# Kernel optimization log

Hardware: AMD Instinct MI355X
Metric: run time of the kernel (lower is better)

The kernel has to match this reference:

```python
import jax, jax.numpy as jnp
import numpy as np

S, B, E = 2048, 2, 768
H = 12
D = E // H  # 64
SCALE = D ** -0.5


def setup_inputs() -> dict:
    key = jax.random.key(0)
    ks = jax.random.split(key, 10)
    inp = {
        "query": jax.random.normal(ks[0], (S, B, E), dtype=jnp.float32),
        "attn_bias": jax.random.normal(ks[1], (B * H, S, S), dtype=jnp.float32) * 0.1,
        "key_padding_mask": jax.random.randint(ks[2], (B, S), 0, 2).astype(bool),
        "Wq": jax.random.normal(ks[3], (E, E), dtype=jnp.float32) * (E ** -0.5),
        "bq": jnp.zeros((E,), dtype=jnp.float32),
        "Wk": jax.random.normal(ks[4], (E, E), dtype=jnp.float32) * (E ** -0.5),
        "bk": jnp.zeros((E,), dtype=jnp.float32),
        "Wv": jax.random.normal(ks[5], (E, E), dtype=jnp.float32) * (E ** -0.5),
        "bv": jnp.zeros((E,), dtype=jnp.float32),
        "Wo": jax.random.normal(ks[6], (E, E), dtype=jnp.float32) * (E ** -0.5),
        "bo": jnp.zeros((E,), dtype=jnp.float32),
    }
    return inp


def reference(query, attn_bias, key_padding_mask, Wq, bq, Wk, bk, Wv, bv, Wo, bo):
    s, b, e = query.shape
    # projections (torch Linear: x @ W.T + b)
    q = (query @ Wq.T + bq) * SCALE
    k = query @ Wk.T + bk
    v = query @ Wv.T + bv
    # [s, b, e] -> [b*h, s, d]
    def to_heads(x):
        return x.reshape(s, b * H, D).transpose(1, 0, 2)
    q, k, v = to_heads(q), to_heads(k), to_heads(v)
    # scores [b*h, s_q, s_k]
    scores = jnp.einsum('nqd,nkd->nqk', q, k) + attn_bias
    # key padding mask: [b, s_k] -> broadcast over heads and queries
    scores = scores.reshape(b, H, s, s)
    scores = jnp.where(key_padding_mask[:, None, None, :], -jnp.inf, scores)
    scores = scores.reshape(b * H, s, s)
    probs = jax.nn.softmax(scores, axis=-1)
    attn = jnp.einsum('nqk,nkd->nqd', probs, v)  # [b*h, s, d]
    attn = attn.transpose(1, 0, 2).reshape(s, b, e)
    return attn @ Wo.T + bo
```

## Files before the change

### kernel.cpp

```cpp
#include <hip/hip_runtime.h>
#include <hip/hip_bf16.h>

typedef __attribute__((ext_vector_type(8))) short s16x8;
typedef __attribute__((ext_vector_type(4))) float f32x4;
typedef unsigned short u16;
typedef unsigned int u32;

#define SDIM 2048
#define BDIM 2
#define HDIM 12
#define DDIM 64
#define EDIM 768
#define MDIM 4096
#define SCALE_Q 0.125f
#define KSPLIT 1024
#define NIT (KSPLIT / 32)
#define HFRAG 131072

static __device__ __forceinline__ f32x4 zero4() {
    f32x4 v; v[0] = v[1] = v[2] = v[3] = 0.f; return v;
}

static __device__ __forceinline__ u16 f2b(float x) {
    u32 u = __builtin_bit_cast(u32, x);
    u32 lsb = (u >> 16) & 1u;
    u += 0x7fffu + lsb;
    return (u16)(u >> 16);
}

static __device__ __forceinline__ f32x4 mfma16(s16x8 a, s16x8 b, f32x4 c) {
    return __builtin_amdgcn_mfma_f32_16x16x32_bf16(a, b, c, 0, 0, 0);
}

static __device__ __forceinline__ void gload_lds16(const void* g, void* l) {
    __builtin_amdgcn_global_load_lds(
        (const __attribute__((address_space(1))) void*)g,
        (__attribute__((address_space(3))) void*)l, 16, 0, 0);
}

__global__ void mask_bits_kernel(const u32* __restrict__ raw, u32* __restrict__ outbits) {
    __shared__ int okInt, okFloat;
    int t = threadIdx.x;
    if (t == 0) { okInt = 1; okFloat = 1; }
    __syncthreads();
    int li = 1, lf = 1;
    for (int i = t; i < 1024; i += blockDim.x) {
        u32 v = raw[i];
        if (v > 1u) li = 0;
        if (v != 0u && v != 0x3F800000u) lf = 0;
    }
    if (!li) atomicAnd(&okInt, 0);
    if (!lf) atomicAnd(&okFloat, 0);
    __syncthreads();
    const unsigned char* rb = (const unsigned char*)raw;
    if (t < (BDIM * SDIM) / 32) {
        u32 bits = 0;
        for (int j = 0; j < 32; ++j) {
            int i = t * 32 + j;
            int v;
            if (okInt)        v = (int)raw[i];
            else if (okFloat) v = (raw[i] != 0u) ? 1 : 0;
            else              v = (int)rb[i];
            bits |= (v ? 1u : 0u) << j;
        }
        outbits[t] = bits;
    }
}

__global__ __launch_bounds__(256) void conv_f32_bf16(
    const float* __restrict__ s, u16* __restrict__ d, int n8)
{
    int i = blockIdx.x * 256 + threadIdx.x;
    if (i >= n8) return;
    float4 x0 = ((const float4*)s)[(size_t)i * 2];
    float4 x1 = ((const float4*)s)[(size_t)i * 2 + 1];
    uint4 o;
    o.x = (u32)f2b(x0.x) | ((u32)f2b(x0.y) << 16);
    o.y = (u32)f2b(x0.z) | ((u32)f2b(x0.w) << 16);
    o.z = (u32)f2b(x1.x) | ((u32)f2b(x1.y) << 16);
    o.w = (u32)f2b(x1.z) | ((u32)f2b(x1.w) << 16);
    ((uint4*)d)[i] = o;
}

__global__ __launch_bounds__(256) void gemm_xwT(
    const u16* __restrict__ A, const u16* __restrict__ Wb,
    const float* __restrict__ bias, float scale,
    u16* __restrict__ out_sc, float* __restrict__ out_rm, int mode)
{
    __shared__ u16 Al[64 * 56];
    __shared__ u16 Bl[64 * 56];
    int tid = threadIdx.x;
    int mb = blockIdx.x * 64, nb = blockIdx.y * 64;
    int lane = tid & 63, w = tid >> 6;
    int r16 = lane & 15, g4 = lane >> 4;
    int wm = w >> 1, wn = w & 1;

    f32x4 acc[2][2];
    acc[0][0] = zero4(); acc[0][1] = zero4(); acc[1][0] = zero4(); acc[1][1] = zero4();

    int srow = tid >> 2, scol = (tid & 3) * 8;

    for (int kb = 0; kb < EDIM; kb += 32) {
        __syncthreads();
        *(uint4*)&Al[srow * 56 + scol] =
            *(const uint4*)&A[(size_t)(mb + srow) * EDIM + kb + scol];
        *(uint4*)&Bl[srow * 56 + scol] =
            *(const uint4*)&Wb[(size_t)(nb + srow) * EDIM + kb + scol];
        __syncthreads();
        s16x8 a[2], bb[2];
        #pragma unroll
        for (int mi = 0; mi < 2; ++mi)
            a[mi] = *(const s16x8*)&Al[(wm * 32 + mi * 16 + r16) * 56 + g4 * 8];
        #pragma unroll
        for (int ni = 0; ni < 2; ++ni)
            bb[ni] = *(const s16x8*)&Bl[(wn * 32 + ni * 16 + r16) * 56 + g4 * 8];
        #pragma unroll
        for (int mi = 0; mi < 2; ++mi)
            #pragma unroll
            for (int ni = 0; ni < 2; ++ni)
                acc[mi][ni] = mfma16(a[mi], bb[ni], acc[mi][ni]);
    }

    #pragma unroll
    for (int mi = 0; mi < 2; ++mi) {
        #pragma unroll
        for (int ni = 0; ni < 2; ++ni) {
            int n = nb + wn * 32 + ni * 16 + r16;
            float bv = bias[n];
            #pragma unroll
            for (int r = 0; r < 4; ++r) {
                int m = mb + wm * 32 + mi * 16 + g4 * 4 + r;
                float c = (acc[mi][ni][r] + bv) * scale;
                if (mode == 1) {
                    int s_ = m >> 1, b_ = m & 1, h_ = n >> 6, d_ = n & 63;
                    out_sc[((size_t)(b_ * HDIM + h_) * SDIM + s_) * DDIM + d_] = f2b(c);
                } else if (mode == 3) {
                    int s_ = m >> 1, b_ = m & 1, h_ = n >> 6, d_ = n & 63;
                    size_t p = (size_t)(b_ * HDIM + h_) * HFRAG
                             + (size_t)(s_ >> 4) * 1024 + (size_t)((d_ >> 5) & 1) * 512
                             + (size_t)(((d_ >> 3) & 3) * 16 + (s_ & 15)) * 8 + (d_ & 7);
                    out_sc[p] = f2b(c);
                } else if (mode == 4) {
                    int s_ = m >> 1, b_ = m & 1, h_ = n >> 6, d_ = n & 63;
                    size_t p = (size_t)(b_ * HDIM + h_) * HFRAG
                             + (size_t)(s_ >> 5) * 2048 + (size_t)((d_ >> 4) & 3) * 512
                             + (size_t)(((s_ >> 3) & 3) * 16 + (d_ & 15)) * 8 + (s_ & 7);
                    out_sc[p] = f2b(c);
                } else {
                    out_rm[(size_t)m * EDIM + n] = c;
                }
            }
        }
    }
}

struct KV { s16x8 k0, k1, k2, k3, v0, v1, v2, v3; };

__global__ __launch_bounds__(128, 4) void attn_fused(
    const u16* __restrict__ qw, const u16* __restrict__ kf_g,
    const u16* __restrict__ vf_g, const float* __restrict__ bias,
    const u32* __restrict__ maskBits, u16* __restrict__ attn_out)
{
    __shared__ __align__(1024) unsigned char SM[18944];

    int qt = blockIdx.x, bh = blockIdx.y;
    int tid = threadIdx.x;
    int w = tid >> 6, lane = tid & 63;
    int r16 = lane & 15, g4 = lane >> 4;
    int qbase = qt * 16;
    int b_ = bh / HDIM, h_ = bh % HDIM;
    const u16* Q  = qw   + (size_t)bh * SDIM * DDIM;
    const u16* KF = kf_g + (size_t)bh * HFRAG;
    const u16* VF = vf_g + (size_t)bh * HFRAG;
    const float* BrowQ = bias + (size_t)bh * SDIM * SDIM + (size_t)qbase * SDIM;
    const u32* mB = maskBits + b_ * (SDIM / 32);

    float* BsW = (float*)(SM + w * 8192);
    u16*   Pl  = (u16*)(SM + 16384 + w * 1280);

    s16x8 qf0 = *(const s16x8*)&Q[(size_t)(qbase + r16) * DDIM + g4 * 8];
    s16x8 qf1 = *(const s16x8*)&Q[(size_t)(qbase + r16) * DDIM + g4 * 8 + 32];

    f32x4 accO[4];
    #pragma unroll
    for (int dt = 0; dt < 4; ++dt) accO[dt] = zero4();
    float m_run = -1e30f, l_run = 0.f;

    const int k0 = w * KSPLIT;

    auto issue_kv = [&](int it, KV& dst) {
        int itc = it < NIT ? it : NIT - 1;
        int kbn = k0 + itc * 32;
        const u16* KT = KF + (size_t)(kbn >> 4) * 1024;
        dst.k0 = *(const s16x8*)&KT[lane * 8];
        dst.k1 = *(const s16x8*)&KT[512 + lane * 8];
        dst.k2 = *(const s16x8*)&KT[1024 + lane * 8];
        dst.k3 = *(const s16x8*)&KT[1536 + lane * 8];
        const u16* VT = VF + (size_t)(kbn >> 5) * 2048;
        dst.v0 = *(const s16x8*)&VT[lane * 8];
        dst.v1 = *(const s16x8*)&VT[512 + lane * 8];
        dst.v2 = *(const s16x8*)&VT[1024 + lane * 8];
        dst.v3 = *(const s16x8*)&VT[1536 + lane * 8];
    };

    auto stage_bias = [&](int it) {
        int itc = it < NIT ? it : NIT - 1;
        int kb2 = k0 + itc * 32;
        float* slot = BsW + (it & 3) * 512;
        #pragma unroll
        for (int j = 0; j < 2; ++j) {
            int sl = j * 64 + lane;
            int row = sl >> 3, q8 = sl & 7;
            int sq = q8 ^ (row & 7);
            gload_lds16(&BrowQ[(size_t)row * SDIM + kb2 + sq * 4],
                        (unsigned char*)slot + j * 1024);
        }
    };

    auto compute = [&](int it, KV& cur) {
        u32 mb = mB[__builtin_amdgcn_readfirstlane((k0 + it * 32) >> 5)];
        f32x4 sc0 = mfma16(cur.k1, qf1, mfma16(cur.k0, qf0, zero4()));
        f32x4 sc1 = mfma16(cur.k3, qf1, mfma16(cur.k2, qf0, zero4()));
        float* Bs = BsW + (it & 3) * 512;
        float4 bc0 = *(const float4*)&Bs[r16 * 32 + ((g4 ^ (r16 & 7)) * 4)];
        float4 bc1 = *(const float4*)&Bs[r16 * 32 + (((4 + g4) ^ (r16 & 7)) * 4)];
        sc0[0] += bc0.x; sc0[1] += bc0.y; sc0[2] += bc0.z; sc0[3] += bc0.w;
        sc1[0] += bc1.x; sc1[1] += bc1.y; sc1[2] += bc1.z; sc1[3] += bc1.w;
        u32 h0 = mb >> (g4 * 4), h1 = mb >> (16 + g4 * 4);
        #pragma unroll
        for (int r = 0; r < 4; ++r) {
            if ((h0 >> r) & 1) sc0[r] = -1e30f;
            if ((h1 >> r) & 1) sc1[r] = -1e30f;
        }
        float pm = fmaxf(fmaxf(fmaxf(sc0[0], sc0[1]), fmaxf(sc0[2], sc0[3])),
                         fmaxf(fmaxf(sc1[0], sc1[1]), fmaxf(sc1[2], sc1[3])));
        pm = fmaxf(pm, __shfl_xor(pm, 16));
        pm = fmaxf(pm, __shfl_xor(pm, 32));
        float mn = fmaxf(m_run, pm);
        float alpha = __expf(m_run - mn);
        float p[8];
        #pragma unroll
        for (int r = 0; r < 4; ++r) p[r]     = __expf(sc0[r] - mn);
        #pragma unroll
        for (int r = 0; r < 4; ++r) p[4 + r] = __expf(sc1[r] - mn);
        float ps = ((p[0] + p[1]) + (p[2] + p[3])) + ((p[4] + p[5]) + (p[6] + p[7]));
        ps += __shfl_xor(ps, 16);
        ps += __shfl_xor(ps, 32);
        l_run = l_run * alpha + ps;
        m_run = mn;
        uint2 pv0, pv1;
        pv0.x = (u32)f2b(p[0]) | ((u32)f2b(p[1]) << 16);
        pv0.y = (u32)f2b(p[2]) | ((u32)f2b(p[3]) << 16);
        pv1.x = (u32)f2b(p[4]) | ((u32)f2b(p[5]) << 16);
        pv1.y = (u32)f2b(p[6]) | ((u32)f2b(p[7]) << 16);
        *(uint2*)&Pl[r16 * 40 + g4 * 4]      = pv0;
        *(uint2*)&Pl[r16 * 40 + 16 + g4 * 4] = pv1;
        float aR0 = __shfl(alpha, g4 * 4 + 0);
        float aR1 = __shfl(alpha, g4 * 4 + 1);
        float aR2 = __shfl(alpha, g4 * 4 + 2);
        float aR3 = __shfl(alpha, g4 * 4 + 3);
        #pragma unroll
        for (int dt = 0; dt < 4; ++dt) {
            accO[dt][0] *= aR0;
            accO[dt][1] *= aR1;
            accO[dt][2] *= aR2;
            accO[dt][3] *= aR3;
        }
        s16x8 pf = *(const s16x8*)&Pl[r16 * 40 + g4 * 8];
        accO[0] = mfma16(pf, cur.v0, accO[0]);
        accO[1] = mfma16(pf, cur.v1, accO[1]);
        accO[2] = mfma16(pf, cur.v2, accO[2]);
        accO[3] = mfma16(pf, cur.v3, accO[3]);
    };

    KV A, B;
    issue_kv(0, A);
    stage_bias(0);
    stage_bias(1);

    for (int t = 0; t < NIT; t += 2) {
        issue_kv(t + 1, B);
        stage_bias(t + 2);
        asm volatile("s_waitcnt vmcnt(12)" ::: "memory");
        __builtin_amdgcn_sched_barrier(0);
        compute(t, A);

        issue_kv(t + 2, A);
        stage_bias(t + 3);
        asm volatile("s_waitcnt vmcnt(12)" ::: "memory");
        __builtin_amdgcn_sched_barrier(0);
        compute(t + 1, B);
    }

    __syncthreads();
    float* As = (float*)SM;
    float* Ml = (float*)(SM + 8704);
    float* Ll = Ml + 32;
    #pragma unroll
    for (int dt = 0; dt < 4; ++dt)
        #pragma unroll
        for (int r = 0; r < 4; ++r)
            As[(w * 16 + g4 * 4 + r) * 68 + dt * 16 + r16] = accO[dt][r];
    if (g4 == 0) { Ml[w * 16 + r16] = m_run; Ll[w * 16 + r16] = l_run; }
    __syncthreads();

    #pragma unroll
    for (int half = 0; half < 2; ++half) {
        int d = w * 32 + half * 16 + r16;
        #pragma unroll
        for (int r = 0; r < 4; ++r) {
            int q = g4 * 4 + r;
            float m0 = Ml[q], m1 = Ml[16 + q];
            float mt = fmaxf(m0, m1);
            float e0 = __expf(m0 - mt), e1 = __expf(m1 - mt);
            float lt = Ll[q] * e0 + Ll[16 + q] * e1;
            float o = (As[q * 68 + d] * e0 + As[(16 + q) * 68 + d] * e1) / lt;
            attn_out[((size_t)(qbase + q) * BDIM + b_) * EDIM + h_ * DDIM + d] = f2b(o);
        }
    }
}

extern "C" void kernel_launch(void* const* d_in, const int* in_sizes, int n_in,
                              void* d_out, int out_size, void* d_ws, size_t ws_size,
                              hipStream_t stream) {
    const float* query     = (const float*)d_in[0];
    const float* attn_bias = (const float*)d_in[1];
    const u32*   mask_raw  = (const u32*)d_in[2];
    const float* Wq = (const float*)d_in[3];
    const float* bq = (const float*)d_in[4];
    const float* Wk = (const float*)d_in[5];
    const float* bk = (const float*)d_in[6];
    const float* Wv = (const float*)d_in[7];
    const float* bv = (const float*)d_in[8];
    const float* Wo = (const float*)d_in[9];
    const float* bo = (const float*)d_in[10];
    float* out = (float*)d_out;

    char* ws = (char*)d_ws;
    u32* maskB = (u32*)ws;
    const size_t HEADSZ = (size_t)BDIM * HDIM * SDIM * DDIM;
    const size_t WSZ = (size_t)EDIM * EDIM;
    u16* qws = (u16*)(ws + 16384);
    u16* kws = qws + HEADSZ;
    u16* vws = kws + HEADSZ;
    u16* aws = vws + HEADSZ;
    u16* qbf = aws;
    u16* wWq = aws + HEADSZ;
    u16* wWk = wWq + WSZ;
    u16* wWv = wWk + WSZ;
    u16* wWo = wWv + WSZ;

    mask_bits_kernel<<<1, 256, 0, stream>>>(mask_raw, maskB);

    conv_f32_bf16<<<(int)(MDIM * EDIM / 8 / 256), 256, 0, stream>>>(query, qbf, MDIM * EDIM / 8);
    conv_f32_bf16<<<(int)(WSZ / 8 / 256), 256, 0, stream>>>(Wq, wWq, (int)(WSZ / 8));
    conv_f32_bf16<<<(int)(WSZ / 8 / 256), 256, 0, stream>>>(Wk, wWk, (int)(WSZ / 8));
    conv_f32_bf16<<<(int)(WSZ / 8 / 256), 256, 0, stream>>>(Wv, wWv, (int)(WSZ / 8));
    conv_f32_bf16<<<(int)(WSZ / 8 / 256), 256, 0, stream>>>(Wo, wWo, (int)(WSZ / 8));

    dim3 gg(MDIM / 64, EDIM / 64);
    gemm_xwT<<<gg, 256, 0, stream>>>(qbf, wWq, bq, SCALE_Q, qws, nullptr, 1);
    gemm_xwT<<<gg, 256, 0, stream>>>(qbf, wWk, bk, 1.0f,    kws, nullptr, 3);
    gemm_xwT<<<gg, 256, 0, stream>>>(qbf, wWv, bv, 1.0f,    vws, nullptr, 4);

    dim3 ga(SDIM / 16, BDIM * HDIM);
    attn_fused<<<ga, 128, 0, stream>>>(qws, kws, vws, attn_bias, maskB, aws);

    gemm_xwT<<<gg, 256, 0, stream>>>(aws, wWo, bo, 1.0f, nullptr, out, 0);
}
```

Baseline: 257.8 us.

## Use single-wave attention blocks with 64-key steps and chunked bias ring

The attention kernel moves from two waves that each handle half the keys and merge at the end to a single wave per 16-query block that walks all keys in 64-key steps. Bias is staged into a double-buffered 256-column LDS ring, one row slice per step, and the cross-wave LDS merge and its syncthreads are removed. This aims to cut merge overhead and per-step softmax bookkeeping and to lengthen the memory pipeline. In exchange each block runs only one wave, the register footprint grows, and occupancy and latency hiding depend on many resident blocks.

```diff
diff --git a/kernel.cpp b/kernel.cpp
--- a/kernel.cpp
+++ b/kernel.cpp
@@ -13,9 +13,9 @@
 #define EDIM 768
 #define MDIM 4096
 #define SCALE_Q 0.125f
-#define KSPLIT 1024
-#define NIT (KSPLIT / 32)
 #define HFRAG 131072
+#define NBODY 32
+#define NCHUNK 8
 
 static __device__ __forceinline__ f32x4 zero4() {
     f32x4 v; v[0] = v[1] = v[2] = v[3] = 0.f; return v;
@@ -154,18 +154,18 @@
     }
 }
 
-struct KV { s16x8 k0, k1, k2, k3, v0, v1, v2, v3; };
-
-__global__ __launch_bounds__(128, 4) void attn_fused(
+struct KV { s16x8 ka[4][2]; s16x8 va[2][4]; };
+
+__global__ __launch_bounds__(64) void attn_fused(
     const u16* __restrict__ qw, const u16* __restrict__ kf_g,
     const u16* __restrict__ vf_g, const float* __restrict__ bias,
     const u32* __restrict__ maskBits, u16* __restrict__ attn_out)
 {
-    __shared__ __align__(1024) unsigned char SM[18944];
+    __shared__ float Ring[2][4096];
+    __shared__ u16 Pl[16 * 72];
 
     int qt = blockIdx.x, bh = blockIdx.y;
-    int tid = threadIdx.x;
-    int w = tid >> 6, lane = tid & 63;
+    int lane = threadIdx.x;
     int r16 = lane & 15, g4 = lane >> 4;
     int qbase = qt * 16;
     int b_ = bh / HDIM, h_ = bh % HDIM;
@@ -175,9 +175,6 @@
     const float* BrowQ = bias + (size_t)bh * SDIM * SDIM + (size_t)qbase * SDIM;
     const u32* mB = maskBits + b_ * (SDIM / 32);
 
-    float* BsW = (float*)(SM + w * 8192);
-    u16*   Pl  = (u16*)(SM + 16384 + w * 1280);
-
     s16x8 qf0 = *(const s16x8*)&Q[(size_t)(qbase + r16) * DDIM + g4 * 8];
     s16x8 qf1 = *(const s16x8*)&Q[(size_t)(qbase + r16) * DDIM + g4 * 8 + 32];
 
@@ -186,75 +183,80 @@
     for (int dt = 0; dt < 4; ++dt) accO[dt] = zero4();
     float m_run = -1e30f, l_run = 0.f;
 
-    const int k0 = w * KSPLIT;
-
-    auto issue_kv = [&](int it, KV& dst) {
-        int itc = it < NIT ? it : NIT - 1;
-        int kbn = k0 + itc * 32;
-        const u16* KT = KF + (size_t)(kbn >> 4) * 1024;
-        dst.k0 = *(const s16x8*)&KT[lane * 8];
-        dst.k1 = *(const s16x8*)&KT[512 + lane * 8];
-        dst.k2 = *(const s16x8*)&KT[1024 + lane * 8];
-        dst.k3 = *(const s16x8*)&KT[1536 + lane * 8];
-        const u16* VT = VF + (size_t)(kbn >> 5) * 2048;
-        dst.v0 = *(const s16x8*)&VT[lane * 8];
-        dst.v1 = *(const s16x8*)&VT[512 + lane * 8];
-        dst.v2 = *(const s16x8*)&VT[1024 + lane * 8];
-        dst.v3 = *(const s16x8*)&VT[1536 + lane * 8];
+    auto issue_kv = [&](int t, KV& dst) {
+        int tc = t < NBODY ? t : NBODY - 1;
+        const u16* KT = KF + (size_t)(tc * 4) * 1024;
+        #pragma unroll
+        for (int kt = 0; kt < 4; ++kt)
+            #pragma unroll
+            for (int c = 0; c < 2; ++c)
+                dst.ka[kt][c] = *(const s16x8*)&KT[kt * 1024 + c * 512 + lane * 8];
+        const u16* VT = VF + (size_t)(tc * 2) * 2048;
+        #pragma unroll
+        for (int ch = 0; ch < 2; ++ch)
+            #pragma unroll
+            for (int dt = 0; dt < 4; ++dt)
+                dst.va[ch][dt] = *(const s16x8*)&VT[ch * 2048 + dt * 512 + lane * 8];
     };
 
-    auto stage_bias = [&](int it) {
-        int itc = it < NIT ? it : NIT - 1;
-        int kb2 = k0 + itc * 32;
-        float* slot = BsW + (it & 3) * 512;
-        #pragma unroll
-        for (int j = 0; j < 2; ++j) {
-            int sl = j * 64 + lane;
-            int row = sl >> 3, q8 = sl & 7;
-            int sq = q8 ^ (row & 7);
-            gload_lds16(&BrowQ[(size_t)row * SDIM + kb2 + sq * 4],
-                        (unsigned char*)slot + j * 1024);
+    auto stage_slice = [&](int t) {
+        int cn = (t >> 2) + 1;
+        int cc = cn < NCHUNK ? cn : NCHUNK - 1;
+        float* slot = Ring[cn & 1];
+        #pragma unroll
+        for (int j = 0; j < 4; ++j) {
+            int q = (t & 3) * 4 + j;
+            gload_lds16(&BrowQ[(size_t)q * SDIM + cc * 256 + ((lane ^ (q & 7)) << 2)],
+                        &slot[q * 256]);
         }
     };
 
-    auto compute = [&](int it, KV& cur) {
-        u32 mb = mB[__builtin_amdgcn_readfirstlane((k0 + it * 32) >> 5)];
-        f32x4 sc0 = mfma16(cur.k1, qf1, mfma16(cur.k0, qf0, zero4()));
-        f32x4 sc1 = mfma16(cur.k3, qf1, mfma16(cur.k2, qf0, zero4()));
-        float* Bs = BsW + (it & 3) * 512;
-        float4 bc0 = *(const float4*)&Bs[r16 * 32 + ((g4 ^ (r16 & 7)) * 4)];
-        float4 bc1 = *(const float4*)&Bs[r16 * 32 + (((4 + g4) ^ (r16 & 7)) * 4)];
-        sc0[0] += bc0.x; sc0[1] += bc0.y; sc0[2] += bc0.z; sc0[3] += bc0.w;
-        sc1[0] += bc1.x; sc1[1] += bc1.y; sc1[2] += bc1.z; sc1[3] += bc1.w;
-        u32 h0 = mb >> (g4 * 4), h1 = mb >> (16 + g4 * 4);
-        #pragma unroll
-        for (int r = 0; r < 4; ++r) {
-            if ((h0 >> r) & 1) sc0[r] = -1e30f;
-            if ((h1 >> r) & 1) sc1[r] = -1e30f;
-        }
-        float pm = fmaxf(fmaxf(fmaxf(sc0[0], sc0[1]), fmaxf(sc0[2], sc0[3])),
-                         fmaxf(fmaxf(sc1[0], sc1[1]), fmaxf(sc1[2], sc1[3])));
+    auto compute = [&](int t, KV& cur) {
+        int b4 = t & 3;
+        const float* Bs = Ring[(t >> 2) & 1];
+        f32x4 sc[4];
+        #pragma unroll
+        for (int kt = 0; kt < 4; ++kt)
+            sc[kt] = mfma16(cur.ka[kt][1], qf1, mfma16(cur.ka[kt][0], qf0, zero4()));
+        u32 mw0 = mB[t * 2], mw1 = mB[t * 2 + 1];
+        #pragma unroll
+        for (int kt = 0; kt < 4; ++kt) {
+            int u = (b4 * 16 + 4 * kt + g4) ^ (r16 & 7);
+            float4 bc = *(const float4*)&Bs[r16 * 256 + u * 4];
+            u32 mseg = ((kt & 2 ? mw1 : mw0) >> (16 * (kt & 1) + 4 * g4)) & 0xF;
+            sc[kt][0] = (mseg & 1) ? -1e30f : sc[kt][0] + bc.x;
+            sc[kt][1] = (mseg & 2) ? -1e30f : sc[kt][1] + bc.y;
+            sc[kt][2] = (mseg & 4) ? -1e30f : sc[kt][2] + bc.z;
+            sc[kt][3] = (mseg & 8) ? -1e30f : sc[kt][3] + bc.w;
+        }
+        float pm = -1e30f;
+        #pragma unroll
+        for (int kt = 0; kt < 4; ++kt)
+            pm = fmaxf(pm, fmaxf(fmaxf(sc[kt][0], sc[kt][1]), fmaxf(sc[kt][2], sc[kt][3])));
         pm = fmaxf(pm, __shfl_xor(pm, 16));
         pm = fmaxf(pm, __shfl_xor(pm, 32));
         float mn = fmaxf(m_run, pm);
         float alpha = __expf(m_run - mn);
-        float p[8];
-        #pragma unroll
-        for (int r = 0; r < 4; ++r) p[r]     = __expf(sc0[r] - mn);
-        #pragma unroll
-        for (int r = 0; r < 4; ++r) p[4 + r] = __expf(sc1[r] - mn);
-        float ps = ((p[0] + p[1]) + (p[2] + p[3])) + ((p[4] + p[5]) + (p[6] + p[7]));
+        float p[16];
+        #pragma unroll
+        for (int kt = 0; kt < 4; ++kt)
+            #pragma unroll
+            for (int r = 0; r < 4; ++r)
+                p[kt * 4 + r] = __expf(sc[kt][r] - mn);
+        float ps = 0.f;
+        #pragma unroll
+        for (int i = 0; i < 16; ++i) ps += p[i];
         ps += __shfl_xor(ps, 16);
         ps += __shfl_xor(ps, 32);
         l_run = l_run * alpha + ps;
         m_run = mn;
-        uint2 pv0, pv1;
-        pv0.x = (u32)f2b(p[0]) | ((u32)f2b(p[1]) << 16);
-        pv0.y = (u32)f2b(p[2]) | ((u32)f2b(p[3]) << 16);
-        pv1.x = (u32)f2b(p[4]) | ((u32)f2b(p[5]) << 16);
-        pv1.y = (u32)f2b(p[6]) | ((u32)f2b(p[7]) << 16);
-        *(uint2*)&Pl[r16 * 40 + g4 * 4]      = pv0;
-        *(uint2*)&Pl[r16 * 40 + 16 + g4 * 4] = pv1;
+        #pragma unroll
+        for (int kt = 0; kt < 4; ++kt) {
+            uint2 pv;
+            pv.x = (u32)f2b(p[kt * 4 + 0]) | ((u32)f2b(p[kt * 4 + 1]) << 16);
+            pv.y = (u32)f2b(p[kt * 4 + 2]) | ((u32)f2b(p[kt * 4 + 3]) << 16);
+            *(uint2*)&Pl[r16 * 72 + kt * 16 + g4 * 4] = pv;
+        }
         float aR0 = __shfl(alpha, g4 * 4 + 0);
         float aR1 = __shfl(alpha, g4 * 4 + 1);
         float aR2 = __shfl(alpha, g4 * 4 + 2);
@@ -266,56 +268,51 @@
             accO[dt][2] *= aR2;
             accO[dt][3] *= aR3;
         }
-        s16x8 pf = *(const s16x8*)&Pl[r16 * 40 + g4 * 8];
-        accO[0] = mfma16(pf, cur.v0, accO[0]);
-        accO[1] = mfma16(pf, cur.v1, accO[1]);
-        accO[2] = mfma16(pf, cur.v2, accO[2]);
-        accO[3] = mfma16(pf, cur.v3, accO[3]);
+        s16x8 pf0 = *(const s16x8*)&Pl[r16 * 72 + g4 * 8];
+        s16x8 pf1 = *(const s16x8*)&Pl[r16 * 72 + 32 + g4 * 8];
+        #pragma unroll
+        for (int dt = 0; dt < 4; ++dt)
+            accO[dt] = mfma16(pf1, cur.va[1][dt], mfma16(pf0, cur.va[0][dt], accO[dt]));
     };
 
     KV A, B;
     issue_kv(0, A);
-    stage_bias(0);
-    stage_bias(1);
-
-    for (int t = 0; t < NIT; t += 2) {
-        issue_kv(t + 1, B);
-        stage_bias(t + 2);
-        asm volatile("s_waitcnt vmcnt(12)" ::: "memory");
+    #pragma unroll
+    for (int q = 0; q < 16; ++q)
+        gload_lds16(&BrowQ[(size_t)q * SDIM + ((lane ^ (q & 7)) << 2)], &Ring[0][q * 256]);
+
+    for (int t4 = 0; t4 < NBODY; t4 += 4) {
+        issue_kv(t4 + 1, B); stage_slice(t4);
+        asm volatile("s_waitcnt vmcnt(20)" ::: "memory");
         __builtin_amdgcn_sched_barrier(0);
-        compute(t, A);
-
-        issue_kv(t + 2, A);
-        stage_bias(t + 3);
-        asm volatile("s_waitcnt vmcnt(12)" ::: "memory");
+        compute(t4, A);
+
+        issue_kv(t4 + 2, A); stage_slice(t4 + 1);
+        asm volatile("s_waitcnt vmcnt(24)" ::: "memory");
         __builtin_amdgcn_sched_barrier(0);
-        compute(t + 1, B);
-    }
-
-    __syncthreads();
-    float* As = (float*)SM;
-    float* Ml = (float*)(SM + 8704);
-    float* Ll = Ml + 32;
-    #pragma unroll
-    for (int dt = 0; dt < 4; ++dt)
-        #pragma unroll
-        for (int r = 0; r < 4; ++r)
-            As[(w * 16 + g4 * 4 + r) * 68 + dt * 16 + r16] = accO[dt][r];
-    if (g4 == 0) { Ml[w * 16 + r16] = m_run; Ll[w * 16 + r16] = l_run; }
-    __syncthreads();
-
-    #pragma unroll
-    for (int half = 0; half < 2; ++half) {
-        int d = w * 32 + half * 16 + r16;
+        compute(t4 + 1, B);
+
+        issue_kv(t4 + 3, B); stage_slice(t4 + 2);
+        asm volatile("s_waitcnt vmcnt(24)" ::: "memory");
+        __builtin_amdgcn_sched_barrier(0);
+        compute(t4 + 2, A);
+
+        issue_kv(t4 + 4, A); stage_slice(t4 + 3);
+        asm volatile("s_waitcnt vmcnt(24)" ::: "memory");
+        __builtin_amdgcn_sched_barrier(0);
+        compute(t4 + 3, B);
+    }
+
+    float lR[4];
+    #pragma unroll
+    for (int r = 0; r < 4; ++r) lR[r] = __shfl(l_run, g4 * 4 + r);
+    #pragma unroll
+    for (int dt = 0; dt < 4; ++dt) {
         #pragma unroll
         for (int r = 0; r < 4; ++r) {
             int q = g4 * 4 + r;
-            float m0 = Ml[q], m1 = Ml[16 + q];
-            float mt = fmaxf(m0, m1);
-            float e0 = __expf(m0 - mt), e1 = __expf(m1 - mt);
-            float lt = Ll[q] * e0 + Ll[16 + q] * e1;
-            float o = (As[q * 68 + d] * e0 + As[(16 + q) * 68 + d] * e1) / lt;
-            attn_out[((size_t)(qbase + q) * BDIM + b_) * EDIM + h_ * DDIM + d] = f2b(o);
+            float o = accO[dt][r] / lR[r];
+            attn_out[((size_t)(qbase + q) * BDIM + b_) * EDIM + h_ * DDIM + dt * 16 + r16] = f2b(o);
         }
     }
 }
@@ -364,7 +361,7 @@
     gemm_xwT<<<gg, 256, 0, stream>>>(qbf, wWv, bv, 1.0f,    vws, nullptr, 4);
 
     dim3 ga(SDIM / 16, BDIM * HDIM);
-    attn_fused<<<ga, 128, 0, stream>>>(qws, kws, vws, attn_bias, maskB, aws);
+    attn_fused<<<ga, 64, 0, stream>>>(qws, kws, vws, attn_bias, maskB, aws);
 
     gemm_xwT<<<gg, 256, 0, stream>>>(aws, wWo, bo, 1.0f, nullptr, out, 0);
 }
```

Result: slower. 270.5 us (+4.9%).

## Process 32 query rows per attention block with lazy rescaling and block swizzle

Applied to the files above, without the earlier changes.

Each attention block now handles 32 query rows instead of 16, so every K/V fragment loaded from global memory feeds two query sub-tiles. The aim is to halve K/V traffic and launch count. The online softmax skips the rescale of the accumulator when no row max grows by more than a threshold, and blocks are remapped with an XCD-style swizzle. The bias ring is cut to two slots with a prefetch distance of one, and the occupancy hint is removed. Costs are more registers and LDS per block, fewer blocks in flight, and a shallower bias prefetch.

```diff
diff --git a/kernel.cpp b/kernel.cpp
--- a/kernel.cpp
+++ b/kernel.cpp
@@ -156,18 +156,21 @@
 
 struct KV { s16x8 k0, k1, k2, k3, v0, v1, v2, v3; };
 
-__global__ __launch_bounds__(128, 4) void attn_fused(
+__global__ __launch_bounds__(128) void attn_fused(
     const u16* __restrict__ qw, const u16* __restrict__ kf_g,
     const u16* __restrict__ vf_g, const float* __restrict__ bias,
     const u32* __restrict__ maskBits, u16* __restrict__ attn_out)
 {
-    __shared__ __align__(1024) unsigned char SM[18944];
-
-    int qt = blockIdx.x, bh = blockIdx.y;
+    __shared__ __align__(1024) unsigned char SM[21504];
+
+    int flat = blockIdx.y * 64 + blockIdx.x;
+    int virt = (flat & 7) * 192 + (flat >> 3);
+    int qt = virt & 63, bh = virt >> 6;
+
     int tid = threadIdx.x;
     int w = tid >> 6, lane = tid & 63;
     int r16 = lane & 15, g4 = lane >> 4;
-    int qbase = qt * 16;
+    int qbase = qt * 32;
     int b_ = bh / HDIM, h_ = bh % HDIM;
     const u16* Q  = qw   + (size_t)bh * SDIM * DDIM;
     const u16* KF = kf_g + (size_t)bh * HFRAG;
@@ -175,22 +178,29 @@
     const float* BrowQ = bias + (size_t)bh * SDIM * SDIM + (size_t)qbase * SDIM;
     const u32* mB = maskBits + b_ * (SDIM / 32);
 
-    float* BsW = (float*)(SM + w * 8192);
-    u16*   Pl  = (u16*)(SM + 16384 + w * 1280);
-
-    s16x8 qf0 = *(const s16x8*)&Q[(size_t)(qbase + r16) * DDIM + g4 * 8];
-    s16x8 qf1 = *(const s16x8*)&Q[(size_t)(qbase + r16) * DDIM + g4 * 8 + 32];
-
-    f32x4 accO[4];
+    unsigned char* wb = SM + w * 10752;
+    float* RingW = (float*)wb;
+    u16*   Pl    = (u16*)(wb + 8192);
+
+    s16x8 qf[2][2];
     #pragma unroll
-    for (int dt = 0; dt < 4; ++dt) accO[dt] = zero4();
-    float m_run = -1e30f, l_run = 0.f;
+    for (int h = 0; h < 2; ++h) {
+        qf[h][0] = *(const s16x8*)&Q[(size_t)(qbase + 16 * h + r16) * DDIM + g4 * 8];
+        qf[h][1] = *(const s16x8*)&Q[(size_t)(qbase + 16 * h + r16) * DDIM + g4 * 8 + 32];
+    }
+
+    f32x4 accO[2][4];
+    #pragma unroll
+    for (int h = 0; h < 2; ++h)
+        #pragma unroll
+        for (int dt = 0; dt < 4; ++dt) accO[h][dt] = zero4();
+    float m_run[2] = {-1e30f, -1e30f}, l_run[2] = {0.f, 0.f};
 
     const int k0 = w * KSPLIT;
 
-    auto issue_kv = [&](int it, KV& dst) {
-        int itc = it < NIT ? it : NIT - 1;
-        int kbn = k0 + itc * 32;
+    auto issue_kv = [&](int t, KV& dst) {
+        int tc = t < NIT ? t : NIT - 1;
+        int kbn = k0 + tc * 32;
         const u16* KT = KF + (size_t)(kbn >> 4) * 1024;
         dst.k0 = *(const s16x8*)&KT[lane * 8];
         dst.k1 = *(const s16x8*)&KT[512 + lane * 8];
@@ -203,119 +213,148 @@
         dst.v3 = *(const s16x8*)&VT[1536 + lane * 8];
     };
 
-    auto stage_bias = [&](int it) {
-        int itc = it < NIT ? it : NIT - 1;
-        int kb2 = k0 + itc * 32;
-        float* slot = BsW + (it & 3) * 512;
-        #pragma unroll
-        for (int j = 0; j < 2; ++j) {
-            int sl = j * 64 + lane;
-            int row = sl >> 3, q8 = sl & 7;
-            int sq = q8 ^ (row & 7);
-            gload_lds16(&BrowQ[(size_t)row * SDIM + kb2 + sq * 4],
-                        (unsigned char*)slot + j * 1024);
+    auto stage_bias = [&](int t) {
+        int tc = t < NIT ? t : NIT - 1;
+        int kb = k0 + tc * 32;
+        unsigned char* slot = (unsigned char*)(RingW + (t & 1) * 1024);
+        int sq = (lane & 7) ^ ((lane >> 3) & 7);
+        #pragma unroll
+        for (int j = 0; j < 4; ++j) {
+            int row = j * 8 + (lane >> 3);
+            gload_lds16(&BrowQ[(size_t)row * SDIM + kb + sq * 4], slot + j * 1024);
         }
     };
 
-    auto compute = [&](int it, KV& cur) {
-        u32 mb = mB[__builtin_amdgcn_readfirstlane((k0 + it * 32) >> 5)];
-        f32x4 sc0 = mfma16(cur.k1, qf1, mfma16(cur.k0, qf0, zero4()));
-        f32x4 sc1 = mfma16(cur.k3, qf1, mfma16(cur.k2, qf0, zero4()));
-        float* Bs = BsW + (it & 3) * 512;
-        float4 bc0 = *(const float4*)&Bs[r16 * 32 + ((g4 ^ (r16 & 7)) * 4)];
-        float4 bc1 = *(const float4*)&Bs[r16 * 32 + (((4 + g4) ^ (r16 & 7)) * 4)];
-        sc0[0] += bc0.x; sc0[1] += bc0.y; sc0[2] += bc0.z; sc0[3] += bc0.w;
-        sc1[0] += bc1.x; sc1[1] += bc1.y; sc1[2] += bc1.z; sc1[3] += bc1.w;
-        u32 h0 = mb >> (g4 * 4), h1 = mb >> (16 + g4 * 4);
-        #pragma unroll
-        for (int r = 0; r < 4; ++r) {
-            if ((h0 >> r) & 1) sc0[r] = -1e30f;
-            if ((h1 >> r) & 1) sc1[r] = -1e30f;
-        }
-        float pm = fmaxf(fmaxf(fmaxf(sc0[0], sc0[1]), fmaxf(sc0[2], sc0[3])),
-                         fmaxf(fmaxf(sc1[0], sc1[1]), fmaxf(sc1[2], sc1[3])));
-        pm = fmaxf(pm, __shfl_xor(pm, 16));
-        pm = fmaxf(pm, __shfl_xor(pm, 32));
-        float mn = fmaxf(m_run, pm);
-        float alpha = __expf(m_run - mn);
-        float p[8];
-        #pragma unroll
-        for (int r = 0; r < 4; ++r) p[r]     = __expf(sc0[r] - mn);
-        #pragma unroll
-        for (int r = 0; r < 4; ++r) p[4 + r] = __expf(sc1[r] - mn);
-        float ps = ((p[0] + p[1]) + (p[2] + p[3])) + ((p[4] + p[5]) + (p[6] + p[7]));
-        ps += __shfl_xor(ps, 16);
-        ps += __shfl_xor(ps, 32);
-        l_run = l_run * alpha + ps;
-        m_run = mn;
-        uint2 pv0, pv1;
-        pv0.x = (u32)f2b(p[0]) | ((u32)f2b(p[1]) << 16);
-        pv0.y = (u32)f2b(p[2]) | ((u32)f2b(p[3]) << 16);
-        pv1.x = (u32)f2b(p[4]) | ((u32)f2b(p[5]) << 16);
-        pv1.y = (u32)f2b(p[6]) | ((u32)f2b(p[7]) << 16);
-        *(uint2*)&Pl[r16 * 40 + g4 * 4]      = pv0;
-        *(uint2*)&Pl[r16 * 40 + 16 + g4 * 4] = pv1;
-        float aR0 = __shfl(alpha, g4 * 4 + 0);
-        float aR1 = __shfl(alpha, g4 * 4 + 1);
-        float aR2 = __shfl(alpha, g4 * 4 + 2);
-        float aR3 = __shfl(alpha, g4 * 4 + 3);
-        #pragma unroll
-        for (int dt = 0; dt < 4; ++dt) {
-            accO[dt][0] *= aR0;
-            accO[dt][1] *= aR1;
-            accO[dt][2] *= aR2;
-            accO[dt][3] *= aR3;
-        }
-        s16x8 pf = *(const s16x8*)&Pl[r16 * 40 + g4 * 8];
-        accO[0] = mfma16(pf, cur.v0, accO[0]);
-        accO[1] = mfma16(pf, cur.v1, accO[1]);
-        accO[2] = mfma16(pf, cur.v2, accO[2]);
-        accO[3] = mfma16(pf, cur.v3, accO[3]);
+    auto compute = [&](int t, KV& cur) {
+        u32 mw = mB[__builtin_amdgcn_readfirstlane((k0 + t * 32) >> 5)];
+        const float* Bs = RingW + (t & 1) * 1024;
+        f32x4 sc[2][2];
+        #pragma unroll
+        for (int h = 0; h < 2; ++h) {
+            sc[h][0] = mfma16(cur.k1, qf[h][1], mfma16(cur.k0, qf[h][0], zero4()));
+            sc[h][1] = mfma16(cur.k3, qf[h][1], mfma16(cur.k2, qf[h][0], zero4()));
+        }
+        #pragma unroll
+        for (int h = 0; h < 2; ++h) {
+            int rr = 16 * h + r16;
+            #pragma unroll
+            for (int kt = 0; kt < 2; ++kt) {
+                float4 bc = *(const float4*)&Bs[rr * 32 + (((4 * kt + g4) ^ (r16 & 7)) * 4)];
+                u32 mseg = (mw >> (16 * kt + 4 * g4)) & 0xF;
+                sc[h][kt][0] = (mseg & 1) ? -1e30f : sc[h][kt][0] + bc.x;
+                sc[h][kt][1] = (mseg & 2) ? -1e30f : sc[h][kt][1] + bc.y;
+                sc[h][kt][2] = (mseg & 4) ? -1e30f : sc[h][kt][2] + bc.z;
+                sc[h][kt][3] = (mseg & 8) ? -1e30f : sc[h][kt][3] + bc.w;
+            }
+        }
+        #pragma unroll
+        for (int h = 0; h < 2; ++h) {
+            float pm = fmaxf(
+                fmaxf(fmaxf(sc[h][0][0], sc[h][0][1]), fmaxf(sc[h][0][2], sc[h][0][3])),
+                fmaxf(fmaxf(sc[h][1][0], sc[h][1][1]), fmaxf(sc[h][1][2], sc[h][1][3])));
+            pm = fmaxf(pm, __shfl_xor(pm, 16));
+            pm = fmaxf(pm, __shfl_xor(pm, 32));
+            bool norescale = __all(pm <= m_run[h] + 4.f);
+            float mn = norescale ? m_run[h] : fmaxf(m_run[h], pm);
+            float p[8];
+            #pragma unroll
+            for (int kt = 0; kt < 2; ++kt)
+                #pragma unroll
+                for (int r = 0; r < 4; ++r)
+                    p[kt * 4 + r] = __expf(sc[h][kt][r] - mn);
+            float ps = ((p[0] + p[1]) + (p[2] + p[3])) + ((p[4] + p[5]) + (p[6] + p[7]));
+            ps += __shfl_xor(ps, 16);
+            ps += __shfl_xor(ps, 32);
+            if (norescale) {
+                l_run[h] += ps;
+            } else {
+                float alpha = __expf(m_run[h] - mn);
+                l_run[h] = l_run[h] * alpha + ps;
+                m_run[h] = mn;
+                float aR0 = __shfl(alpha, g4 * 4 + 0);
+                float aR1 = __shfl(alpha, g4 * 4 + 1);
+                float aR2 = __shfl(alpha, g4 * 4 + 2);
+                float aR3 = __shfl(alpha, g4 * 4 + 3);
+                #pragma unroll
+                for (int dt = 0; dt < 4; ++dt) {
+                    accO[h][dt][0] *= aR0;
+                    accO[h][dt][1] *= aR1;
+                    accO[h][dt][2] *= aR2;
+                    accO[h][dt][3] *= aR3;
+                }
+            }
+            int rr = 16 * h + r16;
+            #pragma unroll
+            for (int kt = 0; kt < 2; ++kt) {
+                uint2 pv;
+                pv.x = (u32)f2b(p[kt * 4 + 0]) | ((u32)f2b(p[kt * 4 + 1]) << 16);
+                pv.y = (u32)f2b(p[kt * 4 + 2]) | ((u32)f2b(p[kt * 4 + 3]) << 16);
+                *(uint2*)&Pl[rr * 40 + kt * 16 + g4 * 4] = pv;
+            }
+        }
+        #pragma unroll
+        for (int h = 0; h < 2; ++h) {
+            s16x8 pf = *(const s16x8*)&Pl[(16 * h + r16) * 40 + g4 * 8];
+            accO[h][0] = mfma16(pf, cur.v0, accO[h][0]);
+            accO[h][1] = mfma16(pf, cur.v1, accO[h][1]);
+            accO[h][2] = mfma16(pf, cur.v2, accO[h][2]);
+            accO[h][3] = mfma16(pf, cur.v3, accO[h][3]);
+        }
     };
 
     KV A, B;
     issue_kv(0, A);
     stage_bias(0);
-    stage_bias(1);
 
     for (int t = 0; t < NIT; t += 2) {
         issue_kv(t + 1, B);
+        stage_bias(t + 1);
+        asm volatile("s_waitcnt vmcnt(12)" ::: "memory");
+        __builtin_amdgcn_sched_barrier(0);
+        compute(t, A);
+
+        issue_kv(t + 2, A);
         stage_bias(t + 2);
         asm volatile("s_waitcnt vmcnt(12)" ::: "memory");
         __builtin_amdgcn_sched_barrier(0);
-        compute(t, A);
-
-        issue_kv(t + 2, A);
-        stage_bias(t + 3);
-        asm volatile("s_waitcnt vmcnt(12)" ::: "memory");
-        __builtin_amdgcn_sched_barrier(0);
         compute(t + 1, B);
     }
 
     __syncthreads();
     float* As = (float*)SM;
-    float* Ml = (float*)(SM + 8704);
-    float* Ll = Ml + 32;
+    float* Ml = (float*)(SM + 17408);
+    float* Ll = Ml + 64;
     #pragma unroll
-    for (int dt = 0; dt < 4; ++dt)
-        #pragma unroll
-        for (int r = 0; r < 4; ++r)
-            As[(w * 16 + g4 * 4 + r) * 68 + dt * 16 + r16] = accO[dt][r];
-    if (g4 == 0) { Ml[w * 16 + r16] = m_run; Ll[w * 16 + r16] = l_run; }
+    for (int h = 0; h < 2; ++h)
+        #pragma unroll
+        for (int dt = 0; dt < 4; ++dt)
+            #pragma unroll
+            for (int r = 0; r < 4; ++r)
+                As[(size_t)(w * 32 + 16 * h + g4 * 4 + r) * 68 + dt * 16 + r16] = accO[h][dt][r];
+    if (g4 == 0) {
+        #pragma unroll
+        for (int h = 0; h < 2; ++h) {
+            Ml[w * 32 + 16 * h + r16] = m_run[h];
+            Ll[w * 32 + 16 * h + r16] = l_run[h];
+        }
+    }
     __syncthreads();
 
     #pragma unroll
-    for (int half = 0; half < 2; ++half) {
-        int d = w * 32 + half * 16 + r16;
-        #pragma unroll
-        for (int r = 0; r < 4; ++r) {
-            int q = g4 * 4 + r;
-            float m0 = Ml[q], m1 = Ml[16 + q];
-            float mt = fmaxf(m0, m1);
-            float e0 = __expf(m0 - mt), e1 = __expf(m1 - mt);
-            float lt = Ll[q] * e0 + Ll[16 + q] * e1;
-            float o = (As[q * 68 + d] * e0 + As[(16 + q) * 68 + d] * e1) / lt;
-            attn_out[((size_t)(qbase + q) * BDIM + b_) * EDIM + h_ * DDIM + d] = f2b(o);
+    for (int h = 0; h < 2; ++h) {
+        #pragma unroll
+        for (int dg = 0; dg < 2; ++dg) {
+            int d = w * 32 + dg * 16 + r16;
+            #pragma unroll
+            for (int r = 0; r < 4; ++r) {
+                int q = 16 * h + g4 * 4 + r;
+                float m0 = Ml[q], m1 = Ml[32 + q];
+                float mt = fmaxf(m0, m1);
+                float e0 = __expf(m0 - mt), e1 = __expf(m1 - mt);
+                float lt = Ll[q] * e0 + Ll[32 + q] * e1;
+                float o = (As[(size_t)q * 68 + d] * e0 + As[(size_t)(32 + q) * 68 + d] * e1) / lt;
+                attn_out[((size_t)(qbase + q) * BDIM + b_) * EDIM + h_ * DDIM + d] = f2b(o);
+            }
         }
     }
 }
@@ -363,7 +402,7 @@
     gemm_xwT<<<gg, 256, 0, stream>>>(qbf, wWk, bk, 1.0f,    kws, nullptr, 3);
     gemm_xwT<<<gg, 256, 0, stream>>>(qbf, wWv, bv, 1.0f,    vws, nullptr, 4);
 
-    dim3 ga(SDIM / 16, BDIM * HDIM);
+    dim3 ga(64, BDIM * HDIM);
     attn_fused<<<ga, 128, 0, stream>>>(qws, kws, vws, attn_bias, maskB, aws);
 
     gemm_xwT<<<gg, 256, 0, stream>>>(aws, wWo, bo, 1.0f, nullptr, out, 0);
```

Measured after the change: 233.3 us. 9.5% less time.
